# Performance work log

Hardware: AMD Instinct MI355X
Metric: run time of the kernel (lower is better)

The kernel has to match this reference:

```python
import jax, jax.numpy as jnp
import numpy as np

N, F_IN, H, C, E = 100000, 128, 128, 40, 600000


def setup_inputs() -> dict:
    key = jax.random.key(0)
    ks = jax.random.split(key, 20)
    s = 0.05
    inp = {
        "x": jax.random.normal(ks[0], (N, F_IN), jnp.float32),
        "edge_index": jax.random.randint(ks[1], (2, E), 0, N, jnp.int64),
        "importance": jnp.ones((F_IN,), jnp.float32),
        "W1": jax.random.normal(ks[2], (H, F_IN), jnp.float32) * s,
        "bl1": jax.random.normal(ks[3], (H,), jnp.float32) * s,
        "bc1": jnp.zeros((H,), jnp.float32),
        "W2": jax.random.normal(ks[4], (H, H), jnp.float32) * s,
        "bl2": jax.random.normal(ks[5], (H,), jnp.float32) * s,
        "bc2": jnp.zeros((H,), jnp.float32),
        "W3": jax.random.normal(ks[6], (H, H), jnp.float32) * s,
        "bl3": jax.random.normal(ks[7], (H,), jnp.float32) * s,
        "bc3": jnp.zeros((H,), jnp.float32),
        "Wlin1": jax.random.normal(ks[8], (H, H), jnp.float32) * s,
        "blin1": jax.random.normal(ks[9], (H,), jnp.float32) * s,
        "Wlin2": jax.random.normal(ks[10], (C, H), jnp.float32) * s,
        "blin2": jax.random.normal(ks[11], (C,), jnp.float32) * s,
    }
    return inp


def balanced_conv(x, W, bl, bc, row, col):
    # lin, then symmetric-normalized message, mean-aggregated over targets
    n = x.shape[0]
    h = x @ W.T + bl                                   # [N, H]
    loops = jnp.arange(n)
    r = jnp.concatenate([row, loops])                  # sources (x_j index)
    c = jnp.concatenate([col, loops])                  # targets
    deg = jnp.zeros((n,), x.dtype).at[c].add(1.0)      # degree(col) incl. self-loops
    dinv = deg ** -0.5
    norm = dinv[r] * dinv[c]                           # [E+N]
    msg = norm[:, None] * h[r]                         # gather + scale
    agg = jnp.zeros((n, h.shape[1]), x.dtype).at[c].add(msg)  # scatter-add
    return agg / deg[:, None] + bc                     # mean aggr + bias


def reference(x, edge_index, importance, W1, bl1, bc1, W2, bl2, bc2,
              W3, bl3, bc3, Wlin1, blin1, Wlin2, blin2):
    row, col = edge_index[0], edge_index[1]
    h = x * importance
    h = jax.nn.relu(balanced_conv(h, W1, bl1, bc1, row, col))
    h = jax.nn.relu(balanced_conv(h, W2, bl2, bc2, row, col))
    h = jax.nn.relu(balanced_conv(h, W3, bl3, bc3, row, col))
    h = jax.nn.relu(h @ Wlin1.T + blin1)
    h = h @ Wlin2.T + blin2
    return jax.nn.log_softmax(h, axis=-1)
```

## Files before the change

### kernel.cpp

```cpp
#include <hip/hip_runtime.h>
#include <hip/hip_bf16.h>

#define F 128
#define C_CLS 40
#define NWSPLIT 35
#define ELLCAP 32

typedef __attribute__((ext_vector_type(8))) short short8;
typedef __attribute__((ext_vector_type(4))) float float4v;
typedef unsigned short ushort;

__device__ inline float bf2f(ushort u) {
  unsigned int x = ((unsigned int)u) << 16;
  return __builtin_bit_cast(float, x);
}
__device__ inline ushort f2bf(float f) {
  __hip_bfloat16 h = __float2bfloat16(f);
  return __builtin_bit_cast(ushort, h);
}
__device__ inline void split_bf16(float f, ushort& hi, ushort& lo) {
  hi = f2bf(f);
  lo = f2bf(f - bf2f(hi));
}
__device__ inline int swz(int lane) { return lane ^ ((lane >> 4) & 3); }

__global__ __launch_bounds__(256) void setup_kernel(
    const float* __restrict__ W1, const float* __restrict__ imp,
    const float* __restrict__ W2, const float* __restrict__ W3,
    const float* __restrict__ Wl1, const float* __restrict__ Wh2,
    ushort* __restrict__ WhP,
    ushort* __restrict__ W2hH, ushort* __restrict__ W2lH,
    const int* __restrict__ row, const int* __restrict__ col,
    int* __restrict__ cnt, int* __restrict__ ell,
    int ne, int n) {
  int b = blockIdx.x;
  if (b < NWSPLIT) {
    int ci = b * 256 + threadIdx.x;
    if (ci < 8192) {
      const float* src[4] = {W1, W2, W3, Wl1};
      int p = ci >> 11, c = ci & 2047;
      int kc = c >> 10, ct = (c >> 7) & 7, ks = (c >> 6) & 1, ln = c & 63;
      int dl = swz(ln);
      int colw = ct * 16 + (dl & 15);
      int k = kc * 64 + ks * 32 + (dl >> 4) * 8;
      float4 f0 = *(const float4*)&src[p][(size_t)colw * F + k];
      float4 f1 = *(const float4*)&src[p][(size_t)colw * F + k + 4];
      float v[8] = {f0.x, f0.y, f0.z, f0.w, f1.x, f1.y, f1.z, f1.w};
      if (p == 0) {
        float4 i0 = *(const float4*)&imp[k];
        float4 i1 = *(const float4*)&imp[k + 4];
        v[0] *= i0.x; v[1] *= i0.y; v[2] *= i0.z; v[3] *= i0.w;
        v[4] *= i1.x; v[5] *= i1.y; v[6] *= i1.z; v[7] *= i1.w;
      }
      ushort hi[8];
#pragma unroll
      for (int j = 0; j < 8; ++j) hi[j] = f2bf(v[j]);
      *(short8*)&WhP[(size_t)ci * 8] = *(short8*)hi;
    } else if (ci < 8192 + 768) {
      int c = ci - 8192;
      int ct = c >> 8, ks = (c >> 6) & 3, ln = c & 63;
      int colw = ct * 16 + (ln & 15);
      int k = ks * 32 + (ln >> 4) * 8;
      float v[8];
      if (colw < C_CLS) {
        float4 f0 = *(const float4*)&Wh2[(size_t)colw * F + k];
        float4 f1 = *(const float4*)&Wh2[(size_t)colw * F + k + 4];
        v[0] = f0.x; v[1] = f0.y; v[2] = f0.z; v[3] = f0.w;
        v[4] = f1.x; v[5] = f1.y; v[6] = f1.z; v[7] = f1.w;
      } else {
#pragma unroll
        for (int j = 0; j < 8; ++j) v[j] = 0.f;
      }
      ushort hi[8], lo[8];
#pragma unroll
      for (int j = 0; j < 8; ++j) split_bf16(v[j], hi[j], lo[j]);
      *(short8*)&W2hH[(size_t)c * 8] = *(short8*)hi;
      *(short8*)&W2lH[(size_t)c * 8] = *(short8*)lo;
    }
  } else {
    int e = (b - NWSPLIT) * 256 + threadIdx.x;
    if (e < ne) {
      int r = row[e], c = col[e];
      int p = atomicAdd(&cnt[c], 1);
      if (p < ELLCAP) ell[(size_t)c * ELLCAP + p] = r;
    }
  }
}

__global__ __launch_bounds__(256) void prepass_kernel(
    const float* __restrict__ x, const int* __restrict__ cnt,
    int* __restrict__ ell, float* __restrict__ wsum,
    ushort* __restrict__ Xs, ushort* __restrict__ Az,
    int n, int nbW, int nbX) {
  int b = blockIdx.x;
  if (b < nbW) {
    int node = b * 256 + threadIdx.x;
    if (node >= n) return;
    int cv = cnt[node];
    int lim = cv < ELLCAP ? cv : ELLCAP;
    int lim4 = (lim + 3) & ~3;
    float gs = 0.f;
    const int4* ep = (const int4*)&ell[(size_t)node * ELLCAP];
    for (int base = 0; base < lim; base += 4) {
      int4 rr = ep[base >> 2];
      bool p1 = base + 1 < lim, p2 = base + 2 < lim, p3 = base + 3 < lim;
      int r1 = p1 ? rr.y : rr.x;
      int r2 = p2 ? rr.z : rr.x;
      int r3 = p3 ? rr.w : rr.x;
      float g0 = rsqrtf((float)(cnt[rr.x] + 1));
      float g1 = p1 ? rsqrtf((float)(cnt[r1] + 1)) : 0.f;
      float g2 = p2 ? rsqrtf((float)(cnt[r2] + 1)) : 0.f;
      float g3 = p3 ? rsqrtf((float)(cnt[r3] + 1)) : 0.f;
      gs += (g0 + g1) + (g2 + g3);
    }
    float d = (float)(cv + 1);
    wsum[node] = rsqrtf(d) * gs + 1.0f / d;
    for (int p = lim; p < lim4; ++p) ell[(size_t)node * ELLCAP + p] = n;
  } else if (b < nbW + nbX) {
    size_t i = (size_t)(b - nbW) * 2048 + (size_t)threadIdx.x * 8;
    if (i < (size_t)n * F) {
      int node = (int)(i >> 7);
      float dc = rsqrtf((float)(cnt[node] + 1));
      float4 f0 = *(const float4*)&x[i];
      float4 f1 = *(const float4*)&x[i + 4];
      ushort o[8] = {f2bf(dc * f0.x), f2bf(dc * f0.y), f2bf(dc * f0.z), f2bf(dc * f0.w),
                     f2bf(dc * f1.x), f2bf(dc * f1.y), f2bf(dc * f1.z), f2bf(dc * f1.w)};
      *(short8*)&Xs[i] = *(short8*)o;
    }
  } else {
    int t = threadIdx.x;
    short8 z = (short8){0, 0, 0, 0, 0, 0, 0, 0};
    if (t < 16) *(short8*)&Xs[(size_t)n * F + t * 8] = z;
    else if (t < 32) *(short8*)&Az[(size_t)n * F + (t - 16) * 8] = z;
  }
}

template <bool SCALE_OUT>
__global__ __launch_bounds__(256) void conv_fused(
    const int* __restrict__ cnt, const int* __restrict__ ell,
    const ushort* __restrict__ Xs, const ushort* __restrict__ Wh,
    const float* __restrict__ wsum, const float* __restrict__ bl,
    const float* __restrict__ bc, ushort* __restrict__ OUT, int n) {
  const int t = threadIdx.x;
  const int w = t >> 6, lane = t & 63, quad = lane >> 4, cl = lane & 15;
  const int node = blockIdx.x * 64 + w * 16 + cl;

  float acc[4][8];
#pragma unroll
  for (int ks = 0; ks < 4; ++ks)
#pragma unroll
    for (int q = 0; q < 8; ++q) acc[ks][q] = 0.f;

  float dc = 1.f, id = 1.f;
  int lim4 = 0;
  if (node < n) {
    int cv = cnt[node];
    float d = (float)(cv + 1);
    dc = rsqrtf(d);
    id = 1.0f / d;
    int lim = cv < ELLCAP ? cv : ELLCAP;
    lim4 = (lim + 3) & ~3;
  }
  const int4* ep = (const int4*)&ell[(size_t)node * ELLCAP];
  const int qoff = quad * 8;

  for (int base = 0; base < lim4; base += 4) {
    int4 rr = ep[base >> 2];
    const ushort* q0 = &Xs[(size_t)rr.x * F + qoff];
    const ushort* q1 = &Xs[(size_t)rr.y * F + qoff];
    const ushort* q2 = &Xs[(size_t)rr.z * F + qoff];
    const ushort* q3 = &Xs[(size_t)rr.w * F + qoff];
#pragma unroll
    for (int ks = 0; ks < 4; ++ks) {
      short8 v0 = *(const short8*)&q0[ks * 32];
      short8 v1 = *(const short8*)&q1[ks * 32];
      short8 v2 = *(const short8*)&q2[ks * 32];
      short8 v3 = *(const short8*)&q3[ks * 32];
#pragma unroll
      for (int q = 0; q < 8; ++q) {
        float t0 = bf2f((ushort)v0[q]) + bf2f((ushort)v1[q]);
        float t1 = bf2f((ushort)v2[q]) + bf2f((ushort)v3[q]);
        acc[ks][q] += t0 + t1;
      }
    }
  }

  short8 sfrag[4];
  if (node < n) {
    const ushort* sq = &Xs[(size_t)node * F + qoff];
#pragma unroll
    for (int ks = 0; ks < 4; ++ks) {
      short8 sv = *(const short8*)&sq[ks * 32];
      ushort o[8];
#pragma unroll
      for (int q = 0; q < 8; ++q)
        o[q] = f2bf(dc * (acc[ks][q] + bf2f((ushort)sv[q])));
      sfrag[ks] = *(short8*)o;
    }
  } else {
#pragma unroll
    for (int ks = 0; ks < 4; ++ks) sfrag[ks] = (short8){0, 0, 0, 0, 0, 0, 0, 0};
  }

  float4v co[8];
#pragma unroll
  for (int mt = 0; mt < 8; ++mt) co[mt] = (float4v){0.f, 0.f, 0.f, 0.f};
  const int sl = swz(lane);
#pragma unroll
  for (int ks = 0; ks < 4; ++ks) {
    const int base2 = ((ks >> 1) * 1024 + (ks & 1) * 64 + sl) * 8;
#pragma unroll
    for (int mt = 0; mt < 8; ++mt) {
      short8 a_h = *(const short8*)&Wh[base2 + mt * 1024];
      co[mt] = __builtin_amdgcn_mfma_f32_16x16x32_bf16(a_h, sfrag[ks], co[mt], 0, 0, 0);
    }
  }

  if (node < n) {
    float ws = wsum[node];
#pragma unroll
    for (int mt = 0; mt < 8; ++mt) {
      float4 blv = *(const float4*)&bl[mt * 16 + quad * 4];
      float4 bcv = *(const float4*)&bc[mt * 16 + quad * 4];
      float v0 = fmaxf((co[mt][0] + ws * blv.x) * id + bcv.x, 0.f);
      float v1 = fmaxf((co[mt][1] + ws * blv.y) * id + bcv.y, 0.f);
      float v2 = fmaxf((co[mt][2] + ws * blv.z) * id + bcv.z, 0.f);
      float v3 = fmaxf((co[mt][3] + ws * blv.w) * id + bcv.w, 0.f);
      if (SCALE_OUT) { v0 *= dc; v1 *= dc; v2 *= dc; v3 *= dc; }
      ushort o[4] = {f2bf(v0), f2bf(v1), f2bf(v2), f2bf(v3)};
      *(ushort4*)&OUT[(size_t)node * F + mt * 16 + quad * 4] = *(ushort4*)o;
    }
  }
}

__global__ __launch_bounds__(256) void head_fused(const ushort* __restrict__ X,
    const ushort* __restrict__ Wl1h, const float* __restrict__ bl,
    const ushort* __restrict__ W2h, const ushort* __restrict__ W2l,
    const float* __restrict__ b2, float* __restrict__ out, int nrows) {
  __shared__ ushort sH[8192];
  __shared__ float b2s[48];
  const int t = threadIdx.x;
  if (t < 48) b2s[t] = (t < C_CLS) ? b2[t] : -1e30f;

  const int w = t >> 6, lane = t & 63;
  const int quad = lane >> 4, cl = lane & 15;
  const int sl = swz(lane);
  const int row0 = (blockIdx.x * 4 + w) * 16;
  char* sHb = (char*)sH;

  float4v acc1[8];
#pragma unroll
  for (int mt = 0; mt < 8; ++mt) acc1[mt] = (float4v){0.f, 0.f, 0.f, 0.f};
  const int gr1 = row0 + cl;
#pragma unroll
  for (int ks = 0; ks < 4; ++ks) {
    short8 b;
    if (gr1 < nrows) b = *(const short8*)&X[(size_t)gr1 * F + ks * 32 + quad * 8];
    else b = (short8){0, 0, 0, 0, 0, 0, 0, 0};
    const int base = ((ks >> 1) * 1024 + (ks & 1) * 64 + sl) * 8;
#pragma unroll
    for (int mt = 0; mt < 8; ++mt) {
      short8 a_h = *(const short8*)&Wl1h[base + mt * 1024];
      acc1[mt] = __builtin_amdgcn_mfma_f32_16x16x32_bf16(a_h, b, acc1[mt], 0, 0, 0);
    }
  }
#pragma unroll
  for (int mt = 0; mt < 8; ++mt) {
    float4 bv = *(const float4*)&bl[mt * 16 + quad * 4];
    ushort o[4];
    o[0] = f2bf(fmaxf(acc1[mt][0] + bv.x, 0.f));
    o[1] = f2bf(fmaxf(acc1[mt][1] + bv.y, 0.f));
    o[2] = f2bf(fmaxf(acc1[mt][2] + bv.z, 0.f));
    o[3] = f2bf(fmaxf(acc1[mt][3] + bv.w, 0.f));
    int ch = (mt * 2 + (quad >> 1)) ^ cl;
    *(ushort4*)&sHb[w * 4096 + cl * 256 + ch * 16 + (quad & 1) * 8] = *(ushort4*)o;
  }
  __syncthreads();

  float4v acc[3];
#pragma unroll
  for (int ct = 0; ct < 3; ++ct) acc[ct] = (float4v){0.f, 0.f, 0.f, 0.f};
#pragma unroll
  for (int ks = 0; ks < 4; ++ks) {
    int ch2 = (ks * 4 + quad) ^ cl;
    short8 a = *(short8*)&sHb[w * 4096 + cl * 256 + ch2 * 16];
#pragma unroll
    for (int ct = 0; ct < 3; ++ct) {
      int chunk = ((ct * 4 + ks) * 64 + lane) * 8;
      short8 b_h = *(const short8*)&W2h[chunk];
      short8 b_l = *(const short8*)&W2l[chunk];
      acc[ct] = __builtin_amdgcn_mfma_f32_16x16x32_bf16(a, b_h, acc[ct], 0, 0, 0);
      acc[ct] = __builtin_amdgcn_mfma_f32_16x16x32_bf16(a, b_l, acc[ct], 0, 0, 0);
    }
  }

  float b0 = b2s[cl], b1 = b2s[16 + cl], b2v = b2s[32 + cl];
  float lse[4];
#pragma unroll
  for (int reg = 0; reg < 4; ++reg) {
    float v0 = acc[0][reg] + b0;
    float v1 = acc[1][reg] + b1;
    float v2 = acc[2][reg] + b2v;
    acc[0][reg] = v0; acc[1][reg] = v1; acc[2][reg] = v2;
    float m = fmaxf(fmaxf(v0, v1), v2);
#pragma unroll
    for (int o = 1; o < 16; o <<= 1) m = fmaxf(m, __shfl_xor(m, o));
    float s = __expf(v0 - m) + __expf(v1 - m) + __expf(v2 - m);
#pragma unroll
    for (int o = 1; o < 16; o <<= 1) s += __shfl_xor(s, o);
    lse[reg] = logf(s) + m;
  }
#pragma unroll
  for (int reg = 0; reg < 4; ++reg) {
    int gr = row0 + quad * 4 + reg;
    if (gr < nrows) {
      out[(size_t)gr * C_CLS + cl] = acc[0][reg] - lse[reg];
      out[(size_t)gr * C_CLS + 16 + cl] = acc[1][reg] - lse[reg];
      if (cl < 8) out[(size_t)gr * C_CLS + 32 + cl] = acc[2][reg] - lse[reg];
    }
  }
}

extern "C" void kernel_launch(void* const* d_in, const int* in_sizes, int n_in,
                              void* d_out, int out_size, void* d_ws, size_t ws_size,
                              hipStream_t stream) {
  const float* x    = (const float*)d_in[0];
  const int*   ei   = (const int*)d_in[1];
  const float* imp  = (const float*)d_in[2];
  const float* W1   = (const float*)d_in[3];
  const float* bl1  = (const float*)d_in[4];
  const float* bc1  = (const float*)d_in[5];
  const float* W2   = (const float*)d_in[6];
  const float* bl2  = (const float*)d_in[7];
  const float* bc2  = (const float*)d_in[8];
  const float* W3   = (const float*)d_in[9];
  const float* bl3  = (const float*)d_in[10];
  const float* bc3  = (const float*)d_in[11];
  const float* Wl1  = (const float*)d_in[12];
  const float* bli1 = (const float*)d_in[13];
  const float* Wl2  = (const float*)d_in[14];
  const float* bli2 = (const float*)d_in[15];
  float* out = (float*)d_out;

  const int N = in_sizes[0] / F;
  const int E = in_sizes[1] / 2;

  ushort* A16 = (ushort*)d_ws;
  ushort* B16 = A16 + (size_t)(N + 1) * F;
  ushort* WhP = B16 + (size_t)(N + 1) * F;
  ushort* W2hH = WhP + 65536;
  ushort* W2lH = W2hH + 6144;
  float* wsum = (float*)(W2lH + 6144);
  int*   cnt  = (int*)(wsum + N);
  int*   ell  = cnt + N;

  const int* rowv = ei;
  const int* colv = ei + E;

  int nbE  = (E + 255) / 256;
  int nbW  = (N + 255) / 256;
  int nbX  = (N * F + 2047) / 2048;
  int nbCv = (N + 63) / 64;
  int nbHd = (N + 63) / 64;

  hipMemsetAsync(cnt, 0, (size_t)N * sizeof(int), stream);
  setup_kernel<<<NWSPLIT + nbE, 256, 0, stream>>>(
      W1, imp, W2, W3, Wl1, Wl2, WhP, W2hH, W2lH, rowv, colv, cnt, ell, E, N);
  prepass_kernel<<<nbW + nbX + 1, 256, 0, stream>>>(
      x, cnt, ell, wsum, B16, A16, N, nbW, nbX);

  conv_fused<true ><<<nbCv, 256, 0, stream>>>(cnt, ell, B16, WhP,         wsum, bl1, bc1, A16, N);
  conv_fused<true ><<<nbCv, 256, 0, stream>>>(cnt, ell, A16, WhP + 16384, wsum, bl2, bc2, B16, N);
  conv_fused<false><<<nbCv, 256, 0, stream>>>(cnt, ell, B16, WhP + 32768, wsum, bl3, bc3, A16, N);

  head_fused<<<nbHd, 256, 0, stream>>>(A16, WhP + 49152, bli1, W2hH, W2lH, bli2, out, N);
}
```

Measured before the change: 347.3 us.

## Sort nodes into degree buckets so conv waves process uniform neighbor counts

Builds a per-bucket histogram of neighbor-iteration counts in the prepass, then a new kernel writes a permutation grouping nodes by bucket, highest degree first. The conv kernels look up their node through this permutation, so lanes in a wave iterate a similar number of times and divergence drops. The gather loop also loads the next ELL index row while the current rows are being summed. The cost is an extra kernel launch, scattered output writes, and lost locality between consecutive nodes.

```diff
diff --git a/kernel.cpp b/kernel.cpp
--- a/kernel.cpp
+++ b/kernel.cpp
@@ -5,6 +5,7 @@
 #define C_CLS 40
 #define NWSPLIT 35
 #define ELLCAP 32
+#define NBKT 9
 
 typedef __attribute__((ext_vector_type(8))) short short8;
 typedef __attribute__((ext_vector_type(4))) float float4v;
@@ -23,6 +24,11 @@
   lo = f2bf(f - bf2f(hi));
 }
 __device__ inline int swz(int lane) { return lane ^ ((lane >> 4) & 3); }
+__device__ inline int bucket_of(int cv) {
+  int lim = cv < ELLCAP ? cv : ELLCAP;
+  int nIt = (lim + 3) >> 2;
+  return 8 - nIt;
+}
 
 __global__ __launch_bounds__(256) void setup_kernel(
     const float* __restrict__ W1, const float* __restrict__ imp,
@@ -89,33 +95,41 @@
 
 __global__ __launch_bounds__(256) void prepass_kernel(
     const float* __restrict__ x, const int* __restrict__ cnt,
-    int* __restrict__ ell, float* __restrict__ wsum,
+    int* __restrict__ ell, float* __restrict__ wsum, int* __restrict__ hist,
     ushort* __restrict__ Xs, ushort* __restrict__ Az,
     int n, int nbW, int nbX) {
   int b = blockIdx.x;
   if (b < nbW) {
-    int node = b * 256 + threadIdx.x;
-    if (node >= n) return;
-    int cv = cnt[node];
-    int lim = cv < ELLCAP ? cv : ELLCAP;
-    int lim4 = (lim + 3) & ~3;
-    float gs = 0.f;
-    const int4* ep = (const int4*)&ell[(size_t)node * ELLCAP];
-    for (int base = 0; base < lim; base += 4) {
-      int4 rr = ep[base >> 2];
-      bool p1 = base + 1 < lim, p2 = base + 2 < lim, p3 = base + 3 < lim;
-      int r1 = p1 ? rr.y : rr.x;
-      int r2 = p2 ? rr.z : rr.x;
-      int r3 = p3 ? rr.w : rr.x;
-      float g0 = rsqrtf((float)(cnt[rr.x] + 1));
-      float g1 = p1 ? rsqrtf((float)(cnt[r1] + 1)) : 0.f;
-      float g2 = p2 ? rsqrtf((float)(cnt[r2] + 1)) : 0.f;
-      float g3 = p3 ? rsqrtf((float)(cnt[r3] + 1)) : 0.f;
-      gs += (g0 + g1) + (g2 + g3);
-    }
-    float d = (float)(cv + 1);
-    wsum[node] = rsqrtf(d) * gs + 1.0f / d;
-    for (int p = lim; p < lim4; ++p) ell[(size_t)node * ELLCAP + p] = n;
+    __shared__ int lh[NBKT];
+    int t = threadIdx.x;
+    if (t < NBKT) lh[t] = 0;
+    __syncthreads();
+    int node = b * 256 + t;
+    if (node < n) {
+      int cv = cnt[node];
+      int lim = cv < ELLCAP ? cv : ELLCAP;
+      int lim4 = (lim + 3) & ~3;
+      float gs = 0.f;
+      const int4* ep = (const int4*)&ell[(size_t)node * ELLCAP];
+      for (int base = 0; base < lim; base += 4) {
+        int4 rr = ep[base >> 2];
+        bool p1 = base + 1 < lim, p2 = base + 2 < lim, p3 = base + 3 < lim;
+        int r1 = p1 ? rr.y : rr.x;
+        int r2 = p2 ? rr.z : rr.x;
+        int r3 = p3 ? rr.w : rr.x;
+        float g0 = rsqrtf((float)(cnt[rr.x] + 1));
+        float g1 = p1 ? rsqrtf((float)(cnt[r1] + 1)) : 0.f;
+        float g2 = p2 ? rsqrtf((float)(cnt[r2] + 1)) : 0.f;
+        float g3 = p3 ? rsqrtf((float)(cnt[r3] + 1)) : 0.f;
+        gs += (g0 + g1) + (g2 + g3);
+      }
+      float d = (float)(cv + 1);
+      wsum[node] = rsqrtf(d) * gs + 1.0f / d;
+      for (int p = lim; p < lim4; ++p) ell[(size_t)node * ELLCAP + p] = n;
+      atomicAdd(&lh[bucket_of(cv)], 1);
+    }
+    __syncthreads();
+    if (t < NBKT) atomicAdd(&hist[t], lh[t]);
   } else if (b < nbW + nbX) {
     size_t i = (size_t)(b - nbW) * 2048 + (size_t)threadIdx.x * 8;
     if (i < (size_t)n * F) {
@@ -135,15 +149,43 @@
   }
 }
 
+__global__ __launch_bounds__(256) void perm_kernel(
+    const int* __restrict__ cnt, const int* __restrict__ hist,
+    int* __restrict__ cursor, int* __restrict__ perm, int n) {
+  __shared__ int lh[NBKT], lbase[NBKT];
+  int t = threadIdx.x;
+  if (t < NBKT) lh[t] = 0;
+  __syncthreads();
+  int node = blockIdx.x * 256 + t;
+  int bkt = 0, idx = 0;
+  if (node < n) {
+    bkt = bucket_of(cnt[node]);
+    idx = atomicAdd(&lh[bkt], 1);
+  }
+  __syncthreads();
+  if (t < NBKT) {
+    int pre = 0;
+#pragma unroll
+    for (int k = 0; k < NBKT; ++k)
+      if (k < t) pre += hist[k];
+    lbase[t] = pre + atomicAdd(&cursor[t], lh[t]);
+  }
+  __syncthreads();
+  if (node < n) perm[lbase[bkt] + idx] = node;
+}
+
 template <bool SCALE_OUT>
 __global__ __launch_bounds__(256) void conv_fused(
     const int* __restrict__ cnt, const int* __restrict__ ell,
+    const int* __restrict__ perm,
     const ushort* __restrict__ Xs, const ushort* __restrict__ Wh,
     const float* __restrict__ wsum, const float* __restrict__ bl,
     const float* __restrict__ bc, ushort* __restrict__ OUT, int n) {
   const int t = threadIdx.x;
   const int w = t >> 6, lane = t & 63, quad = lane >> 4, cl = lane & 15;
-  const int node = blockIdx.x * 64 + w * 16 + cl;
+  const int gid = blockIdx.x * 64 + w * 16 + cl;
+  const bool valid = gid < n;
+  const int node = valid ? perm[gid] : 0;
 
   float acc[4][8];
 #pragma unroll
@@ -152,41 +194,48 @@
     for (int q = 0; q < 8; ++q) acc[ks][q] = 0.f;
 
   float dc = 1.f, id = 1.f;
-  int lim4 = 0;
-  if (node < n) {
+  int nIt = 0;
+  if (valid) {
     int cv = cnt[node];
     float d = (float)(cv + 1);
     dc = rsqrtf(d);
     id = 1.0f / d;
     int lim = cv < ELLCAP ? cv : ELLCAP;
-    lim4 = (lim + 3) & ~3;
+    nIt = (lim + 3) >> 2;
   }
   const int4* ep = (const int4*)&ell[(size_t)node * ELLCAP];
   const int qoff = quad * 8;
 
-  for (int base = 0; base < lim4; base += 4) {
-    int4 rr = ep[base >> 2];
-    const ushort* q0 = &Xs[(size_t)rr.x * F + qoff];
-    const ushort* q1 = &Xs[(size_t)rr.y * F + qoff];
-    const ushort* q2 = &Xs[(size_t)rr.z * F + qoff];
-    const ushort* q3 = &Xs[(size_t)rr.w * F + qoff];
-#pragma unroll
-    for (int ks = 0; ks < 4; ++ks) {
-      short8 v0 = *(const short8*)&q0[ks * 32];
-      short8 v1 = *(const short8*)&q1[ks * 32];
-      short8 v2 = *(const short8*)&q2[ks * 32];
-      short8 v3 = *(const short8*)&q3[ks * 32];
-#pragma unroll
-      for (int q = 0; q < 8; ++q) {
-        float t0 = bf2f((ushort)v0[q]) + bf2f((ushort)v1[q]);
-        float t1 = bf2f((ushort)v2[q]) + bf2f((ushort)v3[q]);
-        acc[ks][q] += t0 + t1;
+  if (nIt > 0) {
+    int4 rr = ep[0];
+    for (int it = 0; it < nIt; ++it) {
+      const ushort* r0 = &Xs[(size_t)rr.x * F + qoff];
+      const ushort* r1 = &Xs[(size_t)rr.y * F + qoff];
+      const ushort* r2 = &Xs[(size_t)rr.z * F + qoff];
+      const ushort* r3 = &Xs[(size_t)rr.w * F + qoff];
+      short8 v[4][4];
+#pragma unroll
+      for (int ks = 0; ks < 4; ++ks) {
+        v[0][ks] = *(const short8*)&r0[ks * 32];
+        v[1][ks] = *(const short8*)&r1[ks * 32];
+        v[2][ks] = *(const short8*)&r2[ks * 32];
+        v[3][ks] = *(const short8*)&r3[ks * 32];
       }
+      int jn = (it + 1 < nIt) ? it + 1 : it;
+      rr = ep[jn];
+#pragma unroll
+      for (int ks = 0; ks < 4; ++ks)
+#pragma unroll
+        for (int q = 0; q < 8; ++q) {
+          float t0 = bf2f((ushort)v[0][ks][q]) + bf2f((ushort)v[1][ks][q]);
+          float t1 = bf2f((ushort)v[2][ks][q]) + bf2f((ushort)v[3][ks][q]);
+          acc[ks][q] += t0 + t1;
+        }
     }
   }
 
   short8 sfrag[4];
-  if (node < n) {
+  if (valid) {
     const ushort* sq = &Xs[(size_t)node * F + qoff];
 #pragma unroll
     for (int ks = 0; ks < 4; ++ks) {
@@ -216,7 +265,7 @@
     }
   }
 
-  if (node < n) {
+  if (valid) {
     float ws = wsum[node];
 #pragma unroll
     for (int mt = 0; mt < 8; ++mt) {
@@ -352,7 +401,10 @@
   ushort* W2lH = W2hH + 6144;
   float* wsum = (float*)(W2lH + 6144);
   int*   cnt  = (int*)(wsum + N);
-  int*   ell  = cnt + N;
+  int*   hist = cnt + N;
+  int*   cursor = hist + NBKT;
+  int*   perm = cursor + NBKT;
+  int*   ell  = perm + N;
 
   const int* rowv = ei;
   const int* colv = ei + E;
@@ -363,15 +415,16 @@
   int nbCv = (N + 63) / 64;
   int nbHd = (N + 63) / 64;
 
-  hipMemsetAsync(cnt, 0, (size_t)N * sizeof(int), stream);
+  hipMemsetAsync(cnt, 0, ((size_t)N + 2 * NBKT) * sizeof(int), stream);
   setup_kernel<<<NWSPLIT + nbE, 256, 0, stream>>>(
       W1, imp, W2, W3, Wl1, Wl2, WhP, W2hH, W2lH, rowv, colv, cnt, ell, E, N);
   prepass_kernel<<<nbW + nbX + 1, 256, 0, stream>>>(
-      x, cnt, ell, wsum, B16, A16, N, nbW, nbX);
-
-  conv_fused<true ><<<nbCv, 256, 0, stream>>>(cnt, ell, B16, WhP,         wsum, bl1, bc1, A16, N);
-  conv_fused<true ><<<nbCv, 256, 0, stream>>>(cnt, ell, A16, WhP + 16384, wsum, bl2, bc2, B16, N);
-  conv_fused<false><<<nbCv, 256, 0, stream>>>(cnt, ell, B16, WhP + 32768, wsum, bl3, bc3, A16, N);
+      x, cnt, ell, wsum, hist, B16, A16, N, nbW, nbX);
+  perm_kernel<<<nbW, 256, 0, stream>>>(cnt, hist, cursor, perm, N);
+
+  conv_fused<true ><<<nbCv, 256, 0, stream>>>(cnt, ell, perm, B16, WhP,         wsum, bl1, bc1, A16, N);
+  conv_fused<true ><<<nbCv, 256, 0, stream>>>(cnt, ell, perm, A16, WhP + 16384, wsum, bl2, bc2, B16, N);
+  conv_fused<false><<<nbCv, 256, 0, stream>>>(cnt, ell, perm, B16, WhP + 32768, wsum, bl3, bc3, A16, N);
 
   head_fused<<<nbHd, 256, 0, stream>>>(A16, WhP + 49152, bli1, W2hH, W2lH, bli2, out, N);
 }
```

Result: faster. 335.7 us (-3.3%).
